# Optimization experiments

Measured on AMD Instinct MI355X. Metric: run time of the kernel, lower is better.

The kernel has to match this reference:

```python
import jax, jax.numpy as jnp
import numpy as np

WS = 8           # window size
NUM_HEADS = 16
DIM = 512
HEAD_DIM = DIM // NUM_HEADS


def _relative_position_index(ws):
    coords = np.stack(np.meshgrid(np.arange(ws), np.arange(ws), indexing='ij'))  # (2, ws, ws)
    cf = coords.reshape(2, -1)                                   # (2, ws*ws)
    rel = cf[:, :, None] - cf[:, None, :]                        # (2, N, N)
    rel = rel.transpose(1, 2, 0).copy()
    rel[:, :, 0] += ws - 1
    rel[:, :, 1] += ws - 1
    rel[:, :, 0] *= 2 * ws - 1
    return jnp.asarray(rel.sum(-1))                              # (N, N) int


REL_IDX = _relative_position_index(WS)


def setup_inputs() -> dict:
    key = jax.random.key(0)
    ks = jax.random.split(key, 4)
    B, C, H, W = 4, DIM, 128, 128
    x = jax.random.normal(ks[0], (B, C, H, W), dtype=jnp.float32)
    gamma = jnp.ones((DIM,), jnp.float32)
    beta = jnp.zeros((DIM,), jnp.float32)
    w_qkv = jax.random.normal(ks[1], (DIM, 3 * DIM), jnp.float32) * (DIM ** -0.5)
    w_proj = jax.random.normal(ks[2], (DIM, DIM), jnp.float32) * (DIM ** -0.5)
    b_proj = jnp.zeros((DIM,), jnp.float32)
    bias_table = jax.random.normal(ks[3], ((2 * WS - 1) ** 2, NUM_HEADS), jnp.float32) * 0.02
    return {"x": x, "gamma": gamma, "beta": beta, "w_qkv": w_qkv,
            "w_proj": w_proj, "b_proj": b_proj, "bias_table": bias_table}


def reference(x, gamma, beta, w_qkv, w_proj, b_proj, bias_table):
    B, C, H, W = x.shape
    pad_h = (WS - H % WS) % WS
    pad_w = (WS - W % WS) % WS
    x = jnp.pad(x, ((0, 0), (0, 0), (0, pad_h), (0, pad_w)))
    Hp, Wp = H + pad_h, W + pad_w
    nh, nw = Hp // WS, Wp // WS
    N = WS * WS  # tokens per window

    # window partition: (B,C,Hp,Wp) -> (B*nh*nw, N, C)
    xw = x.reshape(B, C, nh, WS, nw, WS).transpose(0, 2, 4, 3, 5, 1)
    xw = xw.reshape(B * nh * nw, N, C)

    # LayerNorm over channels
    mu = jnp.mean(xw, axis=-1, keepdims=True)
    var = jnp.var(xw, axis=-1, keepdims=True)
    xn = (xw - mu) * jax.lax.rsqrt(var + 1e-5) * gamma + beta

    # QKV projection (no bias)
    qkv = (xn @ w_qkv).reshape(-1, N, 3, NUM_HEADS, HEAD_DIM)
    qkv = qkv.transpose(2, 0, 3, 1, 4)   # (3, nWin, heads, N, hd)
    q, k, v = qkv[0], qkv[1], qkv[2]

    scale = HEAD_DIM ** -0.5
    attn = jnp.einsum('whnd,whmd->whnm', q, k) * scale          # (nWin, heads, N, N)
    rel_bias = bias_table[REL_IDX]                               # (N, N, heads)
    attn = attn + rel_bias.transpose(2, 0, 1)[None]
    attn = jax.nn.softmax(attn, axis=-1)

    out = jnp.einsum('whnm,whmd->wnhd', attn, v).reshape(-1, N, C)
    out = out @ w_proj + b_proj

    # un-window: (B*nh*nw, N, C) -> (B, C, Hp, Wp)
    out = out.reshape(B, nh, nw, WS, WS, C).transpose(0, 5, 1, 3, 2, 4)
    out = out.reshape(B, C, Hp, Wp)
    return out[:, :, :H, :W]
```

## Files before the change

kernel.cpp:

```cpp
#include <hip/hip_runtime.h>

typedef unsigned short u16;
typedef unsigned int u32;
typedef __bf16 bf16x8 __attribute__((ext_vector_type(8)));
typedef float f32x4 __attribute__((ext_vector_type(4)));

#define C_DIM 512
#define QKV_N 1536
#define KDIM 512
#define NHEAD 16
#define HD 32
#define H_IMG 128
#define W_IMG 128
#define HW 16384
#define NTOK 65536
#define NWIN 1024

#define GLL(g, l) __builtin_amdgcn_global_load_lds( \
    (const __attribute__((address_space(1))) u32*)(g), \
    (__attribute__((address_space(3))) u32*)(l), 16, 0, 0)

#define BAR() __builtin_amdgcn_s_barrier()
#define LGKM0() asm volatile("s_waitcnt lgkmcnt(0)" ::: "memory")
#define VM6() asm volatile("s_waitcnt vmcnt(6)" ::: "memory")
#define VM0() asm volatile("s_waitcnt vmcnt(0)" ::: "memory")

__device__ __forceinline__ u16 f2bf(float f) {
    u32 u = __builtin_bit_cast(u32, f);
    u += 0x7fffu + ((u >> 16) & 1u);
    return (u16)(u >> 16);
}

__global__ void sa_prep_kernel(const float* __restrict__ w_qkv,
                               const float* __restrict__ w_proj,
                               const float* __restrict__ bias_table,
                               u16* __restrict__ wqT, u16* __restrict__ wpT,
                               float* __restrict__ biasP) {
    int t = blockIdx.x * 256 + threadIdx.x;
    const int W1 = KDIM * QKV_N;
    const int W2 = KDIM * C_DIM;
    const int W3 = NHEAD * 64 * 64;
    if (t < W1) {
        int k = t / QKV_N, n = t % QKV_N;
        wqT[n * KDIM + k] = f2bf(w_qkv[t]);
    } else if (t < W1 + W2) {
        int u = t - W1;
        int k = u / C_DIM, n = u % C_DIM;
        wpT[n * KDIM + k] = f2bf(w_proj[u]);
    } else if (t < W1 + W2 + W3) {
        int u = t - W1 - W2;
        int h = u >> 12, n = (u >> 6) & 63, m = u & 63;
        int di = (n >> 3) - (m >> 3) + 7;
        int dj = (n & 7) - (m & 7) + 7;
        biasP[u] = bias_table[(di * 15 + dj) * NHEAD + h];
    }
}

__global__ __launch_bounds__(512, 4) void sa_ln_fused_kernel(const float* __restrict__ x,
        const float* __restrict__ gamma, const float* __restrict__ beta,
        u16* __restrict__ xnc) {
    __shared__ u16 tile[64 * 513];
    __shared__ float ssum[8][64], ssq[8][64];
    __shared__ float smu[64], srs[64];
    int bid = blockIdx.x;
    int win = (bid & 7) * (NWIN / 8) + (bid >> 3);
    int b = win >> 8, wl = win & 255;
    int wh = wl >> 4, ww = wl & 15;
    int tid = threadIdx.x;
    int n = tid & 63;
    int gq = tid >> 6;
    int s_n = (wh * 8 + (n >> 3)) * W_IMG + ww * 8 + (n & 7);
    const float* xb = x + (size_t)b * C_DIM * HW + s_n;
    float sum = 0.f, sq = 0.f;
#pragma unroll 8
    for (int it = 0; it < 64; ++it) {
        int c = it * 8 + gq;
        float v = xb[(size_t)c * HW];
        _Float16 hv = (_Float16)v;
        tile[n * 513 + c] = __builtin_bit_cast(u16, hv);
        sum += v; sq += v * v;
    }
    ssum[gq][n] = sum; ssq[gq][n] = sq;
    __syncthreads();
    if (tid < 64) {
        float S = 0.f, Q = 0.f;
#pragma unroll
        for (int k = 0; k < 8; ++k) { S += ssum[k][n]; Q += ssq[k][n]; }
        float m = S * (1.f / C_DIM);
        float var = Q * (1.f / C_DIM) - m * m;
        smu[n] = m; srs[n] = rsqrtf(var + 1e-5f);
    }
    __syncthreads();
    float gg[8], bb[8];
#pragma unroll
    for (int c0 = 0; c0 < 8; ++c0) { gg[c0] = gamma[c0 * 64 + n]; bb[c0] = beta[c0 * 64 + n]; }
#pragma unroll
    for (int it = 0; it < 8; ++it) {
        int nn = it * 8 + gq;
        float m = smu[nn], r = srs[nn];
        u16* op = xnc + (size_t)((win << 6) + nn) * C_DIM;
#pragma unroll
        for (int c0 = 0; c0 < 8; ++c0) {
            int c = c0 * 64 + n;
            float v = (float)__builtin_bit_cast(_Float16, tile[nn * 513 + c]);
            op[c] = f2bf((v - m) * r * gg[c0] + bb[c0]);
        }
    }
}


#define LDA1(Q,J,KK,BUF) af[Q][J][KK] = *reinterpret_cast<const bf16x8*>( \
    &lds[(BUF)*16384 + (wr*128 + ((Q)*2+(J))*16 + lr)*64 + ((((KK)*4)+lg) ^ (lr & 7))*8])
#define LDAQ(Q,BUF) do{ LDA1(Q,0,0,BUF); LDA1(Q,0,1,BUF); LDA1(Q,1,0,BUF); LDA1(Q,1,1,BUF); }while(0)
#define LDB1(NF,KK,BUF) bfr[NF][KK] = *reinterpret_cast<const bf16x8*>( \
    &lds[32768 + (BUF)*16384 + (wc*64 + (NF)*16 + lr)*64 + ((((KK)*4)+lg) ^ (lr & 7))*8])
#define LDB(BUF) do{ LDB1(0,0,BUF); LDB1(0,1,BUF); LDB1(1,0,BUF); LDB1(1,1,BUF); \
                     LDB1(2,0,BUF); LDB1(2,1,BUF); LDB1(3,0,BUF); LDB1(3,1,BUF); }while(0)
#define MFMA1(M,N,KK) acc[M][N] = __builtin_amdgcn_mfma_f32_16x16x32_bf16(af[(M)/2][(M)&1][KK], bfr[N][KK], acc[M][N], 0, 0, 0)
#define MFMAQ(Q) do{ __builtin_amdgcn_s_setprio(1); \
    MFMA1(2*(Q),0,0);   MFMA1(2*(Q),0,1);   MFMA1(2*(Q),1,0);   MFMA1(2*(Q),1,1); \
    MFMA1(2*(Q),2,0);   MFMA1(2*(Q),2,1);   MFMA1(2*(Q),3,0);   MFMA1(2*(Q),3,1); \
    MFMA1(2*(Q)+1,0,0); MFMA1(2*(Q)+1,0,1); MFMA1(2*(Q)+1,1,0); MFMA1(2*(Q)+1,1,1); \
    MFMA1(2*(Q)+1,2,0); MFMA1(2*(Q)+1,2,1); MFMA1(2*(Q)+1,3,0); MFMA1(2*(Q)+1,3,1); \
    __builtin_amdgcn_s_setprio(0); }while(0)
#define STAGE_A(SRC, KT, H) do{ const u16* _s = (SRC) + (KT)*64 + (size_t)((H)*128)*KDIM; \
    u16* _d = Adst + ((KT)&1)*16384 + (H)*8192; \
    GLL(_s, _d); GLL(_s + (size_t)64*KDIM, _d + 4096); }while(0)
#define STAGE_B(SRC, KT, H) do{ const u16* _s = (SRC) + (KT)*64 + (size_t)((H)*128)*KDIM; \
    u16* _d = Bdst + ((KT)&1)*16384 + (H)*8192; \
    GLL(_s, _d); GLL(_s + (size_t)64*KDIM, _d + 4096); }while(0)
#define PROLOGUE() do{ \
    STAGE_A(Asrc, 0, 0); STAGE_A(Asrc, 0, 1); STAGE_B(Bsrc, 0, 0); STAGE_B(Bsrc, 0, 1); \
    STAGE_B(Bsrc, 1, 0); STAGE_B(Bsrc, 1, 1); STAGE_A(Asrc, 1, 0); \
    VM6(); BAR(); }while(0)

template <int EPI, int R>
__global__ __launch_bounds__(512, 2) void sa_gemm8_kernel(const u16* __restrict__ A,
        const u16* __restrict__ BT, u16* __restrict__ outB, float* __restrict__ outF,
        const float* __restrict__ bias, int nbx, int NT) {
    __shared__ u16 lds[65536];

    const int tid = threadIdx.x;
    const int lane = tid & 63, wv = tid >> 6;
    const int wr = wv >> 2, wc = wv & 3;
    const int lr = lane & 15, lg = lane >> 4;
    const int arow = tid >> 3;
    const int axs = ((tid & 7) ^ ((tid >> 3) & 7)) * 8;
    u16* Adst = lds + tid * 8;
    u16* Bdst = lds + 32768 + tid * 8;

    int mb0, nb0;
    if (R > 1) {
        mb0 = (blockIdx.x & 7) * (256 / 8) + (blockIdx.x >> 3);
        nb0 = 0;
    } else {
        int cpx = gridDim.x >> 3;
        int t = (blockIdx.x & 7) * cpx + (blockIdx.x >> 3);
        mb0 = t / nbx; nb0 = t % nbx;
    }
    const u16* Asrc = A  + (size_t)(mb0 * 256 + arow) * KDIM + axs;
    const u16* Bsrc = BT + (size_t)(nb0 * 256 + arow) * KDIM + axs;

    bf16x8 af[4][2][2];
    bf16x8 bfr[4][2];

    PROLOGUE();

#pragma unroll 1
    for (int r = 0; r < R; ++r) {
        if (EPI == 1 && r > 0) {
            PROLOGUE();
        }
        const bool more = (EPI == 0) && (r + 1 < R);
        const int nbN = (R > 1) ? (r + 1) : nb0;
        const u16* Anext = Asrc;
        const u16* Bnext = BT + (size_t)(nbN * 256 + arow) * KDIM + axs;
        const int m0 = mb0 * 256;
        const int n0 = ((R > 1) ? r : nb0) * 256;

        f32x4 acc[8][4];
#pragma unroll
        for (int i = 0; i < 8; ++i)
#pragma unroll
            for (int j = 0; j < 4; ++j) acc[i][j] = {0.f, 0.f, 0.f, 0.f};

#pragma unroll 1
        for (int i = 0; i < 3; ++i) {
            LDB(0); LDAQ(0, 0); STAGE_A(Asrc, 2*i + 1, 1);
            BAR(); LGKM0(); MFMAQ(0); BAR();
            LDAQ(1, 0); LDAQ(2, 0); STAGE_B(Bsrc, 2*i + 2, 0);
            BAR(); LGKM0(); MFMAQ(1); BAR();
            LDAQ(3, 0); STAGE_B(Bsrc, 2*i + 2, 1);
            BAR(); LGKM0(); MFMAQ(2); BAR();
            STAGE_A(Asrc, 2*i + 2, 0);
            BAR(); LGKM0(); MFMAQ(3); VM6(); BAR();
            LDB(1); LDAQ(0, 1); STAGE_A(Asrc, 2*i + 2, 1);
            BAR(); LGKM0(); MFMAQ(0); BAR();
            LDAQ(1, 1); LDAQ(2, 1); STAGE_B(Bsrc, 2*i + 3, 0);
            BAR(); LGKM0(); MFMAQ(1); BAR();
            LDAQ(3, 1); STAGE_B(Bsrc, 2*i + 3, 1);
            BAR(); LGKM0(); MFMAQ(2); BAR();
            STAGE_A(Asrc, 2*i + 3, 0);
            BAR(); LGKM0(); MFMAQ(3); VM6(); BAR();
        }
        LDB(0); LDAQ(0, 0); STAGE_A(Asrc, 7, 1);
        BAR(); LGKM0(); MFMAQ(0); BAR();
        LDAQ(1, 0); LDAQ(2, 0); if (more) { STAGE_B(Bnext, 0, 0); }
        BAR(); LGKM0(); MFMAQ(1); BAR();
        LDAQ(3, 0); if (more) { STAGE_B(Bnext, 0, 1); }
        BAR(); LGKM0(); MFMAQ(2); BAR();
        if (more) { STAGE_A(Anext, 0, 0); STAGE_A(Anext, 0, 1); }
        BAR(); LGKM0(); MFMAQ(3);
        if (more) { VM6(); } else { VM0(); }
        BAR();
        LDB(1); LDAQ(0, 1);
        BAR(); LGKM0(); MFMAQ(0); BAR();
        LDAQ(1, 1); LDAQ(2, 1); if (more) { STAGE_B(Bnext, 1, 0); STAGE_B(Bnext, 1, 1); }
        BAR(); LGKM0(); MFMAQ(1); BAR();
        LDAQ(3, 1);
        BAR(); LGKM0(); MFMAQ(2); BAR();
        if (more) { STAGE_A(Anext, 1, 0); }
        BAR(); LGKM0(); MFMAQ(3); VM6(); BAR();

        if (EPI == 0) {
#pragma unroll
            for (int mf = 0; mf < 8; ++mf) {
#pragma unroll
                for (int nf = 0; nf < 4; ++nf) {
                    int col = n0 + wc * 64 + nf * 16 + lr;
                    int row = m0 + wr * 128 + mf * 16 + lg * 4;
#pragma unroll
                    for (int rr = 0; rr < 4; ++rr)
                        outB[(size_t)(row + rr) * NT + col] = f2bf(acc[mf][nf][rr]);
                }
            }
        } else {
            int win0 = m0 >> 6;
            int b_img = win0 >> 8, wl = win0 & 255;
            int h0 = (wl >> 4) * 8, w0 = (wl & 15) * 8;
            float* fbuf = reinterpret_cast<float*>(lds);
            __syncthreads();
#pragma unroll
            for (int s = 0; s < 2; ++s) {
                if ((wc >> 1) == s) {
                    int half = wc & 1;
                    float* cb = fbuf + half * 16384;
#pragma unroll
                    for (int mf = 0; mf < 8; ++mf) {
#pragma unroll
                        for (int nf = 0; nf < 4; ++nf) {
                            int cp = nf * 16 + lr;
                            int row = wr * 128 + mf * 16 + lg * 4;
                            int h = (row >> 3) & 7;
                            int sl = ((row >> 6) & 3) * 2 + ((row >> 2) & 1);
                            float bbv = bias[n0 + (2 * s + half) * 64 + cp];
                            f32x4 v = acc[mf][nf];
                            float4 o = {v[0] + bbv, v[1] + bbv, v[2] + bbv, v[3] + bbv};
                            *reinterpret_cast<float4*>(&cb[cp * 256 + h * 32 + (sl ^ (cp & 7)) * 4]) = o;
                        }
                    }
                }
                __syncthreads();
#pragma unroll
                for (int j = 0; j < 16; ++j) {
                    int flat = j * 512 + tid;
                    int half = flat >> 12, f = flat & 4095;
                    int cp = f >> 6, h = (f >> 3) & 7, sl = f & 7;
                    int col = n0 + (2 * s + half) * 64 + cp;
                    float4 v = *reinterpret_cast<const float4*>(
                        &fbuf[half * 16384 + cp * 256 + h * 32 + ((sl ^ (cp & 7))) * 4]);
                    *reinterpret_cast<float4*>(outF + (size_t)(b_img * C_DIM + col) * HW
                                               + (size_t)(h0 + h) * W_IMG + w0 + sl * 4) = v;
                }
                __syncthreads();
            }
        }
        Bsrc = Bnext;
    }
}

__global__ __launch_bounds__(64) void sa_attn_kernel(const u16* __restrict__ qkv,
        const float* __restrict__ biasP, u16* __restrict__ attnc) {
    __shared__ u16 VT[32 * 80];
    __shared__ u16 Ps[64 * 80];
    int bid = blockIdx.x;
    int win  = (bid & 7) * 128 + (bid >> 7);
    int head = (bid >> 3) & 15;
    int lane = threadIdx.x, lr = lane & 15, lg = lane >> 4;
    const u16* base = qkv + (size_t)win * 64 * QKV_N + head * HD;

#pragma unroll
    for (int p = 0; p < 4; ++p) {
        int idx = p * 64 + lane;
        int row = idx >> 2, seg = idx & 3;
        union { uint4 u; u16 s[8]; } cv;
        cv.u = *reinterpret_cast<const uint4*>(base + (size_t)row * QKV_N + 1024 + seg * 8);
#pragma unroll
        for (int e = 0; e < 8; ++e) VT[(seg * 8 + e) * 80 + row] = cv.s[e];
    }

    bf16x8 qa[4], kb[4];
#pragma unroll
    for (int mt = 0; mt < 4; ++mt)
        qa[mt] = *reinterpret_cast<const bf16x8*>(base + (size_t)(mt * 16 + lr) * QKV_N + lg * 8);
#pragma unroll
    for (int nt = 0; nt < 4; ++nt)
        kb[nt] = *reinterpret_cast<const bf16x8*>(base + (size_t)(nt * 16 + lr) * QKV_N + 512 + lg * 8);

    f32x4 sacc[4][4];
#pragma unroll
    for (int i = 0; i < 4; ++i)
#pragma unroll
        for (int j = 0; j < 4; ++j) sacc[i][j] = {0.f, 0.f, 0.f, 0.f};
#pragma unroll
    for (int mt = 0; mt < 4; ++mt)
#pragma unroll
        for (int nt = 0; nt < 4; ++nt)
            sacc[mt][nt] = __builtin_amdgcn_mfma_f32_16x16x32_bf16(qa[mt], kb[nt], sacc[mt][nt], 0, 0, 0);

    __syncthreads();

    const float scale = 0.17677669529663687f;
    const float* bp = biasP + head * 64 * 64;
#pragma unroll
    for (int mt = 0; mt < 4; ++mt) {
#pragma unroll
        for (int rr = 0; rr < 4; ++rr) {
            int row = mt * 16 + lg * 4 + rr;
            float vals[4];
#pragma unroll
            for (int nt = 0; nt < 4; ++nt)
                vals[nt] = sacc[mt][nt][rr] * scale + bp[row * 64 + nt * 16 + lr];
            float mx = fmaxf(fmaxf(vals[0], vals[1]), fmaxf(vals[2], vals[3]));
#pragma unroll
            for (int d = 1; d < 16; d <<= 1) mx = fmaxf(mx, __shfl_xor(mx, d, 64));
            float sm = 0.f;
#pragma unroll
            for (int nt = 0; nt < 4; ++nt) { vals[nt] = __expf(vals[nt] - mx); sm += vals[nt]; }
#pragma unroll
            for (int d = 1; d < 16; d <<= 1) sm += __shfl_xor(sm, d, 64);
            float inv = 1.f / sm;
#pragma unroll
            for (int nt = 0; nt < 4; ++nt)
                Ps[row * 80 + nt * 16 + lr] = f2bf(vals[nt] * inv);
        }
    }
    __syncthreads();

    f32x4 oacc[4][2];
#pragma unroll
    for (int i = 0; i < 4; ++i) { oacc[i][0] = {0.f,0.f,0.f,0.f}; oacc[i][1] = {0.f,0.f,0.f,0.f}; }
#pragma unroll
    for (int ks = 0; ks < 2; ++ks) {
        bf16x8 pa[4], vb[2];
#pragma unroll
        for (int mt = 0; mt < 4; ++mt)
            pa[mt] = *reinterpret_cast<const bf16x8*>(&Ps[(mt * 16 + lr) * 80 + ks * 32 + lg * 8]);
#pragma unroll
        for (int n2 = 0; n2 < 2; ++n2)
            vb[n2] = *reinterpret_cast<const bf16x8*>(&VT[(n2 * 16 + lr) * 80 + ks * 32 + lg * 8]);
#pragma unroll
        for (int mt = 0; mt < 4; ++mt)
#pragma unroll
            for (int n2 = 0; n2 < 2; ++n2)
                oacc[mt][n2] = __builtin_amdgcn_mfma_f32_16x16x32_bf16(pa[mt], vb[n2], oacc[mt][n2], 0, 0, 0);
    }

#pragma unroll
    for (int mt = 0; mt < 4; ++mt)
#pragma unroll
        for (int n2 = 0; n2 < 2; ++n2)
#pragma unroll
            for (int rr = 0; rr < 4; ++rr) {
                int row = mt * 16 + lg * 4 + rr;
                attnc[(size_t)(win * 64 + row) * C_DIM + head * HD + n2 * 16 + lr] =
                    f2bf(oacc[mt][n2][rr]);
            }
}

extern "C" void kernel_launch(void* const* d_in, const int* in_sizes, int n_in,
                              void* d_out, int out_size, void* d_ws, size_t ws_size,
                              hipStream_t stream) {
    const float* x          = (const float*)d_in[0];
    const float* gamma      = (const float*)d_in[1];
    const float* beta       = (const float*)d_in[2];
    const float* w_qkv      = (const float*)d_in[3];
    const float* w_proj     = (const float*)d_in[4];
    const float* b_proj     = (const float*)d_in[5];
    const float* bias_table = (const float*)d_in[6];
    float* out = (float*)d_out;

    char* ws = (char*)d_ws;
    size_t off = 0;
    auto alloc = [&](size_t bytes) {
        char* p = ws + off;
        off += (bytes + 255) & ~(size_t)255;
        return p;
    };
    u16*   wqT   = (u16*)alloc((size_t)KDIM * QKV_N * 2);
    u16*   wpT   = (u16*)alloc((size_t)KDIM * C_DIM * 2);
    float* biasP = (float*)alloc((size_t)NHEAD * 64 * 64 * 4);
    u16*   xnc   = (u16*)alloc((size_t)NTOK * C_DIM * 2);
    u16*   qkvc  = (u16*)alloc((size_t)NTOK * QKV_N * 2);
    u16*   attnc = (u16*)alloc((size_t)NTOK * C_DIM * 2);

    sa_prep_kernel<<<4352, 256, 0, stream>>>(w_qkv, w_proj, bias_table, wqT, wpT, biasP);
    sa_ln_fused_kernel<<<NWIN, 512, 0, stream>>>(x, gamma, beta, xnc);
    sa_gemm8_kernel<0, 1><<<256 * 6, 512, 0, stream>>>(xnc, wqT, qkvc, nullptr, nullptr, 6, QKV_N);
    sa_attn_kernel<<<NWIN * NHEAD, 64, 0, stream>>>(qkvc, biasP, attnc);
    sa_gemm8_kernel<1, 2><<<256, 512, 0, stream>>>(attnc, wpT, nullptr, out, b_proj, 2, C_DIM);
}
```

Measured before the change: 336.6 us.

## Process two tiles per block in QKV GEMM and load V directly in attention

```diff
diff --git a/kernel.cpp b/kernel.cpp
--- a/kernel.cpp
+++ b/kernel.cpp
@@ -137,7 +137,7 @@
 template <int EPI, int R>
 __global__ __launch_bounds__(512, 2) void sa_gemm8_kernel(const u16* __restrict__ A,
         const u16* __restrict__ BT, u16* __restrict__ outB, float* __restrict__ outF,
-        const float* __restrict__ bias, int nbx, int NT) {
+        const float* __restrict__ bias, int NT) {
     __shared__ u16 lds[65536];
 
     const int tid = threadIdx.x;
@@ -149,34 +149,26 @@
     u16* Adst = lds + tid * 8;
     u16* Bdst = lds + 32768 + tid * 8;
 
-    int mb0, nb0;
-    if (R > 1) {
-        mb0 = (blockIdx.x & 7) * (256 / 8) + (blockIdx.x >> 3);
-        nb0 = 0;
-    } else {
-        int cpx = gridDim.x >> 3;
-        int t = (blockIdx.x & 7) * cpx + (blockIdx.x >> 3);
-        mb0 = t / nbx; nb0 = t % nbx;
-    }
-    const u16* Asrc = A  + (size_t)(mb0 * 256 + arow) * KDIM + axs;
-    const u16* Bsrc = BT + (size_t)(nb0 * 256 + arow) * KDIM + axs;
+    const int cpx = gridDim.x >> 3;
+    const int g = (blockIdx.x & 7) * cpx + (blockIdx.x >> 3);
+    const int tile0 = g * R;
 
     bf16x8 af[4][2][2];
     bf16x8 bfr[4][2];
 
-    PROLOGUE();
-
 #pragma unroll 1
     for (int r = 0; r < R; ++r) {
-        if (EPI == 1 && r > 0) {
-            PROLOGUE();
-        }
+        const int t = tile0 + r;
+        const int mb = t & 255, nb = t >> 8;
+        const int tn = t + 1;
+        const u16* Asrc = A  + (size_t)(mb * 256 + arow) * KDIM + axs;
+        const u16* Bsrc = BT + (size_t)(nb * 256 + arow) * KDIM + axs;
+        const u16* Anext = A  + (size_t)((tn & 255) * 256 + arow) * KDIM + axs;
+        const u16* Bnext = BT + (size_t)((tn >> 8) * 256 + arow) * KDIM + axs;
+        const int m0 = mb * 256, n0 = nb * 256;
         const bool more = (EPI == 0) && (r + 1 < R);
-        const int nbN = (R > 1) ? (r + 1) : nb0;
-        const u16* Anext = Asrc;
-        const u16* Bnext = BT + (size_t)(nbN * 256 + arow) * KDIM + axs;
-        const int m0 = mb0 * 256;
-        const int n0 = ((R > 1) ? r : nb0) * 256;
+
+        if (r == 0 || EPI == 1) { PROLOGUE(); }
 
         f32x4 acc[8][4];
 #pragma unroll
@@ -275,13 +267,11 @@
                 __syncthreads();
             }
         }
-        Bsrc = Bnext;
     }
 }
 
 __global__ __launch_bounds__(64) void sa_attn_kernel(const u16* __restrict__ qkv,
         const float* __restrict__ biasP, u16* __restrict__ attnc) {
-    __shared__ u16 VT[32 * 80];
     __shared__ u16 Ps[64 * 80];
     int bid = blockIdx.x;
     int win  = (bid & 7) * 128 + (bid >> 7);
@@ -289,16 +279,6 @@
     int lane = threadIdx.x, lr = lane & 15, lg = lane >> 4;
     const u16* base = qkv + (size_t)win * 64 * QKV_N + head * HD;
 
-#pragma unroll
-    for (int p = 0; p < 4; ++p) {
-        int idx = p * 64 + lane;
-        int row = idx >> 2, seg = idx & 3;
-        union { uint4 u; u16 s[8]; } cv;
-        cv.u = *reinterpret_cast<const uint4*>(base + (size_t)row * QKV_N + 1024 + seg * 8);
-#pragma unroll
-        for (int e = 0; e < 8; ++e) VT[(seg * 8 + e) * 80 + row] = cv.s[e];
-    }
-
     bf16x8 qa[4], kb[4];
 #pragma unroll
     for (int mt = 0; mt < 4; ++mt)
@@ -318,7 +298,14 @@
         for (int nt = 0; nt < 4; ++nt)
             sacc[mt][nt] = __builtin_amdgcn_mfma_f32_16x16x32_bf16(qa[mt], kb[nt], sacc[mt][nt], 0, 0, 0);
 
-    __syncthreads();
+    union { u16 s[8]; bf16x8 v; } vb[2][2];
+#pragma unroll
+    for (int ks = 0; ks < 2; ++ks)
+#pragma unroll
+        for (int n2 = 0; n2 < 2; ++n2)
+#pragma unroll
+            for (int i = 0; i < 8; ++i)
+                vb[ks][n2].s[i] = base[(size_t)(ks * 32 + lg * 8 + i) * QKV_N + 1024 + n2 * 16 + lr];
 
     const float scale = 0.17677669529663687f;
     const float* bp = biasP + head * 64 * 64;
@@ -352,18 +339,15 @@
     for (int i = 0; i < 4; ++i) { oacc[i][0] = {0.f,0.f,0.f,0.f}; oacc[i][1] = {0.f,0.f,0.f,0.f}; }
 #pragma unroll
     for (int ks = 0; ks < 2; ++ks) {
-        bf16x8 pa[4], vb[2];
+        bf16x8 pa[4];
 #pragma unroll
         for (int mt = 0; mt < 4; ++mt)
             pa[mt] = *reinterpret_cast<const bf16x8*>(&Ps[(mt * 16 + lr) * 80 + ks * 32 + lg * 8]);
 #pragma unroll
-        for (int n2 = 0; n2 < 2; ++n2)
-            vb[n2] = *reinterpret_cast<const bf16x8*>(&VT[(n2 * 16 + lr) * 80 + ks * 32 + lg * 8]);
-#pragma unroll
         for (int mt = 0; mt < 4; ++mt)
 #pragma unroll
             for (int n2 = 0; n2 < 2; ++n2)
-                oacc[mt][n2] = __builtin_amdgcn_mfma_f32_16x16x32_bf16(pa[mt], vb[n2], oacc[mt][n2], 0, 0, 0);
+                oacc[mt][n2] = __builtin_amdgcn_mfma_f32_16x16x32_bf16(pa[mt], vb[ks][n2].v, oacc[mt][n2], 0, 0, 0);
     }
 
 #pragma unroll
@@ -406,7 +390,7 @@
 
     sa_prep_kernel<<<4352, 256, 0, stream>>>(w_qkv, w_proj, bias_table, wqT, wpT, biasP);
     sa_ln_fused_kernel<<<NWIN, 512, 0, stream>>>(x, gamma, beta, xnc);
-    sa_gemm8_kernel<0, 1><<<256 * 6, 512, 0, stream>>>(xnc, wqT, qkvc, nullptr, nullptr, 6, QKV_N);
+    sa_gemm8_kernel<0, 2><<<768, 512, 0, stream>>>(xnc, wqT, qkvc, nullptr, nullptr, QKV_N);
     sa_attn_kernel<<<NWIN * NHEAD, 64, 0, stream>>>(qkvc, biasP, attnc);
-    sa_gemm8_kernel<1, 2><<<256, 512, 0, stream>>>(attnc, wpT, nullptr, out, b_proj, 2, C_DIM);
-}
+    sa_gemm8_kernel<1, 2><<<256, 512, 0, stream>>>(attnc, wpT, nullptr, out, b_proj, C_DIM);
+}
```

New measurement: 403.2 us. +19.8%, slower.
